# Performance work log

Hardware: AMD Instinct MI355X
Metric: run time of the kernel (lower is better)

The kernel has to match this reference:

```python
import jax, jax.numpy as jnp
import numpy as np

B, L = 64, 200
NQ = 1024          # n_question == output_dim
NPID = 4096
D = 256            # q_embed_dim
H = 512            # hidden_dim
Q = 1024           # output_dim
L2 = 1e-05


def setup_inputs() -> dict:
    key = jax.random.key(0)
    ks = jax.random.split(key, 20)
    q_data = jax.random.randint(ks[0], (B, L), 1, NQ + 1)          # question ids in [1, NQ]
    ans = jax.random.randint(ks[1], (B, L), 0, 2)
    qa_data = q_data + NQ * ans                                     # encoded (q, answer)
    pid_data = jax.random.randint(ks[2], (B, L), 0, NPID + 1)
    matrix = jax.random.uniform(ks[3], (Q, Q), jnp.float32) * 0.05  # p_c_relations
    u = jax.random.uniform(ks[4], (B, L))
    target = jnp.where(u < 0.1, -1.0, jnp.where(u < 0.55, 0.0, 1.0)).astype(jnp.float32)
    s = 0.05
    q_emb = jax.random.normal(ks[5], (NQ + 1, D), jnp.float32) * s
    qa_emb = jax.random.normal(ks[6], (2, D), jnp.float32) * s
    q_emb_diff = jax.random.normal(ks[7], (NQ + 1, D), jnp.float32) * s
    qa_emb_diff = jax.random.normal(ks[8], (2 * NQ + 1, D), jnp.float32) * s
    diff_parm = jax.random.normal(ks[9], (NPID + 1, 1), jnp.float32) * s
    gs = 1.0 / np.sqrt(H).astype(np.float32)
    w_ih = jax.random.uniform(ks[10], (3 * H, 2 * D), jnp.float32, -gs, gs)
    w_hh = jax.random.uniform(ks[11], (3 * H, H), jnp.float32, -gs, gs)
    b_ih = jax.random.uniform(ks[12], (3 * H,), jnp.float32, -gs, gs)
    b_hh = jax.random.uniform(ks[13], (3 * H,), jnp.float32, -gs, gs)
    fc_w = jax.random.normal(ks[14], (Q, H), jnp.float32) * 0.02
    fc_b = jnp.zeros((Q,), jnp.float32)
    return dict(q_data=q_data, qa_data=qa_data, pid_data=pid_data, matrix=matrix,
                target=target, q_emb=q_emb, qa_emb=qa_emb, q_emb_diff=q_emb_diff,
                qa_emb_diff=qa_emb_diff, diff_parm=diff_parm, w_ih=w_ih, w_hh=w_hh,
                b_ih=b_ih, b_hh=b_hh, fc_w=fc_w, fc_b=fc_b)


def _gru(x, w_ih, w_hh, b_ih, b_hh):
    # PyTorch GRU, single layer, batch_first. x: [B, L, In]
    xg = jnp.einsum('bli,gi->blg', x, w_ih) + b_ih          # [B, L, 3H]
    def step(h, xg_t):
        hg = h @ w_hh.T + b_hh
        xr, xz, xn = jnp.split(xg_t, 3, axis=-1)
        hr, hz, hn = jnp.split(hg, 3, axis=-1)
        r = jax.nn.sigmoid(xr + hr)
        z = jax.nn.sigmoid(xz + hz)
        n = jnp.tanh(xn + r * hn)
        h_new = (1.0 - z) * n + z * h
        return h_new, h_new
    h0 = jnp.zeros((x.shape[0], w_hh.shape[1]), x.dtype)
    _, hs = jax.lax.scan(step, h0, xg.transpose(1, 0, 2))
    return hs.transpose(1, 0, 2)                             # [B, L, H]


def reference(q_data, qa_data, pid_data, matrix, target, q_emb, qa_emb,
              q_emb_diff, qa_emb_diff, diff_parm, w_ih, w_hh, b_ih, b_hh,
              fc_w, fc_b):
    q_embed = q_emb[q_data]                                  # [B, L, D]
    qa = (qa_data - q_data) // NQ                            # answer in {0,1}
    qa_embed = qa_emb[qa] + q_embed
    pid_embed = diff_parm[pid_data]                          # [B, L, 1]
    q_embed2 = q_embed + pid_embed * q_emb_diff[q_data]
    qa_embed2 = qa_embed + pid_embed * qa_emb_diff[qa]
    c_reg = (pid_embed ** 2).sum() * L2

    x = jnp.concatenate([qa_embed2, q_embed2], axis=-1)      # [B, L, 2D]
    gru_out = _gru(x, w_ih, w_hh, b_ih, b_hh)
    gru_out = jnp.einsum('blh,qh->blq', gru_out, fc_w) + fc_b  # [B, L, Q]

    got = jnp.einsum('blq,kq->blk', gru_out, matrix)         # [B, L, Q]
    master = jnp.where(got >= 0.4, 1.0, got)                 # threshold-to-1 only
    # mastery of the question asked at step t: master[b, t, q-1]
    mvals = jnp.take_along_axis(master, (q_data - 1)[..., None], axis=2)[..., 0]  # [B, L]

    f32 = jnp.float32
    eq = (q_data[:, :, None] == q_data[:, None, :]).astype(f32)   # [B, t, k]
    t_idx = jnp.arange(L)
    tri_strict = (t_idx[:, None] > t_idx[None, :]).astype(f32)    # k < t
    tri_incl = (t_idx[:, None] >= t_idx[None, :]).astype(f32)     # k <= t
    mast = (mvals == 1.0).astype(f32)
    notm = (mvals == 0.0).astype(f32)
    qa1 = (qa == 1).astype(f32)
    qa0 = 1.0 - qa1
    base = eq * tri_strict                                        # [B, L, L]
    mc = jnp.einsum('btk,bk->bt', base, qa1 * mast)   # master_correct
    mi = jnp.einsum('btk,bk->bt', base, qa0 * mast)   # master_incorrect
    nmc = jnp.einsum('btk,bk->bt', base, qa0 * notm)  # no_master_correct
    aa = jnp.einsum('btk,tk->bt', eq, tri_incl)       # answered_all (>= 1)

    arB = jnp.arange(B)
    idx = q_data - 1

    def dina_step(carry, xs):
        guess, slip = carry                            # [B, Q] each
        i_t, m_t, qa_t, mc_t, mi_t, nmc_t, aa_t = xs   # [B] each
        g_upd = jnp.where(m_t == 1.0, mc_t / aa_t,
                          jnp.where(qa_t == 0, 1.0 - nmc_t / aa_t, nmc_t / aa_t))
        upd_slip = (m_t == 1.0) & (qa_t == 0)
        new_g = jnp.where(upd_slip, guess[arB, i_t], g_upd)
        new_s = jnp.where(upd_slip, mi_t / aa_t, slip[arB, i_t])
        guess = guess.at[arB, i_t].set(new_g)
        slip = slip.at[arB, i_t].set(new_s)
        p = (1.0 - new_s) * (m_t * new_g + (1.0 - new_s) * (1.0 - m_t))
        return (guess, slip), p

    init = (jnp.zeros((B, Q), f32), jnp.zeros((B, Q), f32))
    xs = (idx.T, mvals.T, qa.T, mc.T, mi.T, nmc.T, aa.T)
    _, ps = jax.lax.scan(dina_step, init, xs)          # [L, B]
    preds = ps.T.reshape(-1)                           # [B*L]

    labels = target.reshape(-1)
    mask = labels > -0.9
    preds_d = jax.lax.stop_gradient(preds)             # torch detaches via torch.tensor()
    mse_sum = (((preds_d - labels) ** 2) * mask.astype(f32)).sum()
    loss = mse_sum + c_reg
    return (loss, jax.nn.sigmoid(preds_d), mask.sum())
```

## Files before the change

kernel.cpp:

```cpp
#include <hip/hip_runtime.h>
#include <hip/hip_bf16.h>
#include <math.h>

#define BB 64
#define LL 200
#define NQ 1024
#define DD 256
#define HH 512
#define QQ 1024
#define G3 1536
#define BL 12800
#define GBLK 256

#define OFF_ACC   ((size_t)0)
#define OFF_CELLS ((size_t)16)
#define OFF_HA    ((size_t)1056)
#define OFF_AQ    (OFF_HA + 65536)
#define OFF_DQ    (OFF_AQ + 1574400)
#define OFF_BQA   (OFF_DQ + 1574400)
#define OFF_CQA   (OFF_BQA + 3072)
#define OFF_WSUM  (OFF_CQA + 3072)
#define OFF_FCWT  (OFF_WSUM + 393216)
#define OFF_M2    (OFF_FCWT + 524288)
#define OFF_MB    (OFF_M2 + 524288)
#define OFF_XG    (OFF_MB + 1024)
#define OFF_GRUT  (OFF_XG + 19660800)
#define OFF_QINT  (OFF_GRUT + 6553600)
#define OFF_QAINT (OFF_QINT + 12800)
#define OFF_PIDF  (OFF_QAINT + 12800)
#define OFF_MVAL  (OFF_PIDF + 12800)
#define OFF_MC    (OFF_MVAL + 12800)
#define OFF_MI    (OFF_MC + 12800)
#define OFF_NMC   (OFF_MI + 12800)
#define OFF_AA    (OFF_NMC + 12800)
#define OFF_PREDS (OFF_AA + 12800)

typedef float f32x4 __attribute__((ext_vector_type(4)));

__device__ __forceinline__ float wave_sum64(float v) {
    #pragma unroll
    for (int o = 32; o > 0; o >>= 1) v += __shfl_down(v, o, 64);
    return v;
}

__device__ __forceinline__ f32x4 llc_load4(const float* p) {
    f32x4 v;
    asm volatile("global_load_dwordx4 %0, %1, off sc0 sc1" : "=v"(v) : "v"(p));
    return v;
}
__device__ __forceinline__ void llc_wait2(f32x4& a, f32x4& b) {
    asm volatile("s_waitcnt vmcnt(0)" : "+v"(a), "+v"(b));
}
__device__ __forceinline__ void llc_store1(float* p, float v) {
    asm volatile("global_store_dword %0, %1, off sc0 sc1" :: "v"(p), "v"(v) : "memory");
}

__device__ __forceinline__ float quad_sum(float v) {
    float t1 = __int_as_float(__builtin_amdgcn_update_dpp(
        0, __float_as_int(v), 0xB1, 0xF, 0xF, true));
    v += t1;
    float t2 = __int_as_float(__builtin_amdgcn_update_dpp(
        0, __float_as_int(v), 0x4E, 0xF, 0xF, true));
    return v + t2;
}

__global__ __launch_bounds__(256) void wsum_kernel(const float* __restrict__ w_ih,
                                                   float* __restrict__ wsum)
{
    int g = blockIdx.x, d = threadIdx.x;
    wsum[(size_t)g * DD + d] = w_ih[(size_t)g * 2 * DD + d] + w_ih[(size_t)g * 2 * DD + DD + d];
}

__device__ __forceinline__ void gemm_nt_body(
    const float* __restrict__ A, int lda, const float* __restrict__ B, int ldb,
    float* __restrict__ C, int ldc, int M, int N, int K,
    const float* __restrict__ bias, int bm, int bn, int tid,
    float (*As)[129], float (*Bs)[65])
{
    const int tx = tid & 15, ty = tid >> 4;
    const int mm = tid >> 4, kk = tid & 15;
    float acc[8][4] = {};
    float ar[8], br[4];
    #pragma unroll
    for (int i = 0; i < 8; ++i) {
        int m = bm + mm + 16 * i;
        ar[i] = (m < M) ? A[(size_t)m * lda + kk] : 0.f;
    }
    #pragma unroll
    for (int i = 0; i < 4; ++i) {
        int n = bn + mm + 16 * i;
        br[i] = (n < N) ? B[(size_t)n * ldb + kk] : 0.f;
    }
    for (int k0 = 0; k0 < K; k0 += 16) {
        #pragma unroll
        for (int i = 0; i < 8; ++i) As[kk][mm + 16 * i] = ar[i];
        #pragma unroll
        for (int i = 0; i < 4; ++i) Bs[kk][mm + 16 * i] = br[i];
        __syncthreads();
        int kn = k0 + 16;
        if (kn < K) {
            #pragma unroll
            for (int i = 0; i < 8; ++i) {
                int m = bm + mm + 16 * i;
                ar[i] = (m < M) ? A[(size_t)m * lda + kn + kk] : 0.f;
            }
            #pragma unroll
            for (int i = 0; i < 4; ++i) {
                int n = bn + mm + 16 * i;
                br[i] = (n < N) ? B[(size_t)n * ldb + kn + kk] : 0.f;
            }
        }
        #pragma unroll
        for (int kq = 0; kq < 16; ++kq) {
            float a[8], b[4];
            #pragma unroll
            for (int i = 0; i < 8; ++i) a[i] = As[kq][ty * 8 + i];
            #pragma unroll
            for (int j = 0; j < 4; ++j) b[j] = Bs[kq][tx * 4 + j];
            #pragma unroll
            for (int i = 0; i < 8; ++i)
                #pragma unroll
                for (int j = 0; j < 4; ++j) acc[i][j] += a[i] * b[j];
        }
        __syncthreads();
    }
    #pragma unroll
    for (int i = 0; i < 8; ++i) {
        int m = bm + ty * 8 + i;
        if (m >= M) continue;
        #pragma unroll
        for (int j = 0; j < 4; ++j) {
            int n = bn + tx * 4 + j;
            if (n >= N) continue;
            C[(size_t)m * ldc + n] = acc[i][j] + (bias ? bias[n] : 0.f);
        }
    }
}

__global__ __launch_bounds__(256) void prep_all(
    const float* __restrict__ q_emb, const float* __restrict__ q_emb_diff,
    const float* __restrict__ qa_emb, const float* __restrict__ qa_emb_diff,
    const float* __restrict__ wsum, const float* __restrict__ w_ih,
    const float* __restrict__ b_ih,
    float* __restrict__ Aq, float* __restrict__ Dq,
    float* __restrict__ Bqa, float* __restrict__ Cqa,
    const float* __restrict__ matrix, const float* __restrict__ fc_w,
    const float* __restrict__ fc_b, float* __restrict__ M2, float* __restrict__ mb,
    const int* __restrict__ q_data, const int* __restrict__ qa_data,
    const int* __restrict__ pid_data, const float* __restrict__ diff_parm,
    int* __restrict__ qint, int* __restrict__ qaint, float* __restrict__ pidf,
    float* __restrict__ acc_g)
{
    __shared__ float As[16][129];
    __shared__ float Bs[16][65];
    __shared__ float sm[4];
    const int tid = threadIdx.x;
    const int widx = blockIdx.x;

    if (widx < 432) {
        const int z = widx >= 216;
        const int w2 = z ? widx - 216 : widx;
        const int bm = (w2 / 24) * 128, bn = (w2 % 24) * 64;
        gemm_nt_body(z ? q_emb_diff : q_emb, DD,
                     z ? (w_ih + DD) : wsum, z ? 2 * DD : DD,
                     z ? Dq : Aq, G3, NQ + 1, G3, DD,
                     nullptr, bm, bn, tid, As, Bs);
        return;
    }
    if (widx < 480) {
        const int w2 = widx - 432;
        const int z = w2 >= 24;
        const int bn = (z ? w2 - 24 : w2) * 64;
        gemm_nt_body(z ? qa_emb_diff : qa_emb, DD,
                     w_ih, 2 * DD,
                     z ? Cqa : Bqa, G3, 2, G3, DD,
                     z ? nullptr : b_ih, 0, bn, tid, As, Bs);
        return;
    }
    if (widx < 608) {
        const int w2 = widx - 480;
        const int bm = (w2 >> 3) * 64, bn = (w2 & 7) * 64;
        const int kk = tid & 15, mm = tid >> 4;
        const int nb = tid & 63, kb2 = tid >> 6;
        const int tx = tid & 15, ty = tid >> 4;
        float acc[4][4] = {};
        for (int k0 = 0; k0 < QQ; k0 += 16) {
            if (k0) __syncthreads();
            #pragma unroll
            for (int i = 0; i < 4; ++i)
                As[kk][mm + 16 * i] = matrix[(size_t)(bm + mm + 16 * i) * QQ + k0 + kk];
            #pragma unroll
            for (int i = 0; i < 4; ++i)
                Bs[kb2 + 4 * i][nb] = fc_w[(size_t)(k0 + kb2 + 4 * i) * HH + bn + nb];
            __syncthreads();
            #pragma unroll
            for (int kq = 0; kq < 16; ++kq) {
                float a[4], b[4];
                #pragma unroll
                for (int i = 0; i < 4; ++i) a[i] = As[kq][ty * 4 + i];
                #pragma unroll
                for (int j = 0; j < 4; ++j) b[j] = Bs[kq][tx * 4 + j];
                #pragma unroll
                for (int i = 0; i < 4; ++i)
                    #pragma unroll
                    for (int j = 0; j < 4; ++j) acc[i][j] += a[i] * b[j];
            }
        }
        #pragma unroll
        for (int i = 0; i < 4; ++i)
            #pragma unroll
            for (int j = 0; j < 4; ++j)
                M2[(size_t)(bm + ty * 4 + i) * HH + bn + tx * 4 + j] = acc[i][j];
        return;
    }
    if (widx < 612) {
        const int wv2 = tid >> 6, lane2 = tid & 63;
        const int kb = (widx - 608) * 256 + wv2 * 64;
        for (int i = 0; i < 64; ++i) {
            const float* mrow = matrix + (size_t)(kb + i) * QQ;
            float sacc = 0.f;
            #pragma unroll
            for (int j = 0; j < 16; ++j)
                sacc += mrow[lane2 + 64 * j] * fc_b[lane2 + 64 * j];
            sacc = wave_sum64(sacc);
            if (lane2 == 0) mb[kb + i] = sacc;
        }
        return;
    }
    {
        int r = (widx - 612) * 256 + tid;
        float pp = 0.f;
        if (r < BL) {
            int q = q_data[r];
            qint[r] = q;
            qaint[r] = (qa_data[r] - q) / NQ;
            float pid = diff_parm[pid_data[r]];
            pidf[r] = pid;
            pp = pid * pid;
        }
        pp = wave_sum64(pp);
        int lane = tid & 63, w = tid >> 6;
        if (lane == 0) sm[w] = pp;
        __syncthreads();
        if (tid == 0) atomicAdd(&acc_g[0], sm[0] + sm[1] + sm[2] + sm[3]);
    }
}

__global__ __launch_bounds__(512) void gru_persist(
    const float* __restrict__ Aq,
    const float* __restrict__ Dq,
    const float* __restrict__ Bqa,
    const float* __restrict__ Cqa,
    const int* __restrict__ qint,
    const int* __restrict__ qaint,
    const float* __restrict__ pidf,
    const float* __restrict__ w_hh,
    const float* __restrict__ b_hh,
    float* __restrict__ hA,
    float* __restrict__ gruT2,
    unsigned int* __restrict__ cells)
{
    __shared__ float hs[8][512];
    __shared__ float part[8][3][16][8];
    __shared__ float bqs[2][3][16];
    __shared__ float cqs[2][3][16];
    __shared__ int smq[8][200];
    __shared__ int smqa[8][200];
    __shared__ float smp[8][200];

    const int tid = threadIdx.x;
    const int bid = blockIdx.x;
    const int bg = bid >> 5;
    const int j0 = (bid & 31) * 16;
    const int wv = tid >> 6;
    const int lane = tid & 63;
    const int g = lane >> 2;
    const int s = lane & 3;

    if (tid < 96) {
        const int qa = tid / 48, rem = tid - qa * 48;
        const int gate = rem >> 4, u = rem & 15;
        bqs[qa][gate][u] = Bqa[(size_t)qa * G3 + gate * HH + j0 + u];
        cqs[qa][gate][u] = Cqa[(size_t)qa * G3 + gate * HH + j0 + u];
    }
    for (int i = tid; i < 8 * LL; i += 512) {
        const int c = i / LL, tt = i - c * LL;
        const int col = bg * 8 + c;
        smq[c][tt] = qint[col * LL + tt];
        smqa[c][tt] = qaint[col * LL + tt];
        smp[c][tt] = pidf[col * LL + tt];
    }

    f32x4 ws4[3][4];
    #pragma unroll
    for (int gate = 0; gate < 3; ++gate)
        #pragma unroll
        for (int q = 0; q < 4; ++q)
            ws4[gate][q] = *(const f32x4*)&w_hh[
                (size_t)(gate * HH + j0 + g) * HH + wv * 64 + q * 16 + s * 4];

    const int eu = tid >> 3;
    const int eb = tid & 7;
    float bhr = 0.f, bhz = 0.f, bhn = 0.f;
    if (tid < 128) {
        bhr = b_hh[j0 + eu];
        bhz = b_hh[HH + j0 + eu];
        bhn = b_hh[2 * HH + j0 + eu];
    }

    const int b0 = lane >> 4;
    const int c0 = (lane & 15) * 4;

    __syncthreads();

    for (int t = 0; t < LL; ++t) {
        float xr = 0.f, xz = 0.f, xn = 0.f;
        if (tid < 128) {
            const int q = smq[eb][t];
            const int qa = smqa[eb][t];
            const float pid = smp[eb][t];
            const float* aq = Aq + (size_t)q * G3 + j0 + eu;
            const float* dq = Dq + (size_t)q * G3 + j0 + eu;
            float ar_ = aq[0], az_ = aq[HH], an_ = aq[2 * HH];
            float dr_ = dq[0], dz_ = dq[HH], dn_ = dq[2 * HH];
            xr = ar_ + bqs[qa][0][eu] + pid * (cqs[qa][0][eu] + dr_);
            xz = az_ + bqs[qa][1][eu] + pid * (cqs[qa][1][eu] + dz_);
            xn = an_ + bqs[qa][2][eu] + pid * (cqs[qa][2][eu] + dn_);
        }
        if (t && tid < 64) {
            const unsigned want = (unsigned)t;
            for (;;) {
                unsigned v = want;
                if (lane < 32)
                    v = __hip_atomic_load(&cells[(bg * 32 + lane) * 4],
                                          __ATOMIC_RELAXED, __HIP_MEMORY_SCOPE_AGENT);
                if (__all((int)(v >= want))) break;
                __builtin_amdgcn_s_sleep(2);
            }
        }
        __syncthreads();

        {
            const float* hcur = hA + (size_t)(t & 1) * (HH * BB);
            const float* p0 = hcur + (size_t)(bg * 8 + b0) * HH + wv * 64 + c0;
            f32x4 va = llc_load4(p0);
            f32x4 vb = llc_load4(p0 + 4 * HH);
            llc_wait2(va, vb);
            *(f32x4*)&hs[wv][b0 * 64 + ((c0 + 8 * b0) & 63)] = va;
            *(f32x4*)&hs[wv][(b0 + 4) * 64 + ((c0 + 8 * b0 + 32) & 63)] = vb;
        }

        float acc[3][8];
        #pragma unroll
        for (int gate = 0; gate < 3; ++gate) {
            #pragma unroll
            for (int b = 0; b < 8; ++b) acc[gate][b] = 0.f;
        }
        #pragma unroll
        for (int q = 0; q < 4; ++q) {
            const int cb = q * 16 + s * 4;
            #pragma unroll
            for (int b = 0; b < 8; ++b) {
                f32x4 h4 = *(const f32x4*)&hs[wv][b * 64 + ((cb + 8 * b) & 63)];
                #pragma unroll
                for (int gate = 0; gate < 3; ++gate) {
                    acc[gate][b] += ws4[gate][q].x * h4.x + ws4[gate][q].y * h4.y
                                  + ws4[gate][q].z * h4.z + ws4[gate][q].w * h4.w;
                }
            }
        }

        #pragma unroll
        for (int gate = 0; gate < 3; ++gate)
            #pragma unroll
            for (int b = 0; b < 8; ++b)
                acc[gate][b] = quad_sum(acc[gate][b]);

        if (s < 3) {
            const int rot = (2 * ((g >> 2) + s)) & 7;
            #pragma unroll
            for (int hp = 0; hp < 4; ++hp) {
                const int b = hp * 2;
                float e0 = (s == 0) ? acc[0][b]     : (s == 1) ? acc[1][b]     : acc[2][b];
                float e1 = (s == 0) ? acc[0][b + 1] : (s == 1) ? acc[1][b + 1] : acc[2][b + 1];
                const int bp = (b + rot) & 7;
                *(float2*)&part[wv][s][g][bp] = make_float2(e0, e1);
            }
        }
        __syncthreads();

        if (tid < 128) {
            const int rb = eu >> 2;
            const int bp0 = (eb + 2 * (rb + 0)) & 7;
            const int bp1 = (eb + 2 * (rb + 1)) & 7;
            const int bp2 = (eb + 2 * (rb + 2)) & 7;
            float sg0 = 0.f, sg1 = 0.f, sg2 = 0.f;
            #pragma unroll
            for (int w = 0; w < 8; ++w) {
                sg0 += part[w][0][eu][bp0];
                sg1 += part[w][1][eu][bp1];
                sg2 += part[w][2][eu][bp2];
            }
            const int ku = j0 + eu;
            float hprev = hs[ku >> 6][eb * 64 + (((ku & 63) + 8 * eb) & 63)];
            float rg = 1.f / (1.f + expf(-(xr + sg0 + bhr)));
            float zg = 1.f / (1.f + expf(-(xz + sg1 + bhz)));
            float ng = tanhf(xn + rg * (sg2 + bhn));
            float hn = (1.f - zg) * ng + zg * hprev;
            llc_store1(hA + (size_t)((t + 1) & 1) * (HH * BB)
                          + (size_t)(bg * 8 + eb) * HH + ku, hn);
            gruT2[((size_t)t * BB + bg * 8 + eb) * HH + ku] = hn;
            asm volatile("s_waitcnt vmcnt(0)" ::: "memory");
        }
        __syncthreads();
        if (tid == 0 && t + 1 < LL)
            __hip_atomic_store(&cells[bid * 4], (unsigned)(t + 1),
                               __ATOMIC_RELAXED, __HIP_MEMORY_SCOPE_AGENT);
    }
}

__global__ __launch_bounds__(256) void mval_kernel(
    const float* __restrict__ gruT2,
    const float* __restrict__ M2,
    const float* __restrict__ mb,
    const int* __restrict__ qint,
    float* __restrict__ mval)
{
    int t = blockIdx.x;
    int wave = threadIdx.x >> 6, l = threadIdx.x & 63;
    for (int ii = 0; ii < 16; ++ii) {
        int b = wave * 16 + ii;
        int q = qint[b * LL + t] - 1;
        const float4* hp = (const float4*)(gruT2 + ((size_t)t * BB + b) * HH);
        const float4* mp = (const float4*)(M2 + (size_t)q * HH);
        float4 h0 = hp[l], m0 = mp[l];
        float4 h1 = hp[64 + l], m1 = mp[64 + l];
        float acc = h0.x * m0.x + h0.y * m0.y + h0.z * m0.z + h0.w * m0.w
                  + h1.x * m1.x + h1.y * m1.y + h1.z * m1.z + h1.w * m1.w;
        acc = wave_sum64(acc);
        if (l == 0) {
            float sv = acc + mb[q];
            mval[b * LL + t] = (sv >= 0.4f) ? 1.0f : sv;
        }
    }
}

__global__ __launch_bounds__(256) void statsdina_kernel(
    const int* __restrict__ qint, const int* __restrict__ qaint,
    const float* __restrict__ mval, float* __restrict__ preds)
{
    int b = blockIdx.x, tid = threadIdx.x;
    __shared__ float guess[QQ], slip[QQ];
    __shared__ int qs[LL];
    __shared__ int qas[LL];
    __shared__ float mv[LL], s_mc[LL], s_mi[LL], s_nmc[LL], s_aa[LL];
    for (int i = tid; i < QQ; i += 256) { guess[i] = 0.f; slip[i] = 0.f; }
    if (tid < LL) {
        qs[tid] = qint[b * LL + tid];
        qas[tid] = qaint[b * LL + tid];
        mv[tid] = mval[b * LL + tid];
    }
    __syncthreads();
    if (tid < LL) {
        int qt = qs[tid];
        float smc = 0.f, smi = 0.f, snmc = 0.f, saa = 0.f;
        for (int k = 0; k <= tid; ++k) {
            if (qs[k] == qt) {
                saa += 1.f;
                if (k < tid) {
                    float mk = (mv[k] == 1.f) ? 1.f : 0.f;
                    float nk = (mv[k] == 0.f) ? 1.f : 0.f;
                    float a1 = (qas[k] == 1) ? 1.f : 0.f;
                    smc += a1 * mk;
                    smi += (1.f - a1) * mk;
                    snmc += (1.f - a1) * nk;
                }
            }
        }
        s_mc[tid] = smc;
        s_mi[tid] = smi;
        s_nmc[tid] = snmc;
        s_aa[tid] = saa;
    }
    __syncthreads();
    if (tid == 0) {
        for (int t = 0; t < LL; ++t) {
            int i = qs[t] - 1;
            float m = mv[t];
            int qa = qas[t];
            float aat = s_aa[t];
            float g_upd = (m == 1.f) ? s_mc[t] / aat
                          : ((qa == 0) ? 1.f - s_nmc[t] / aat : s_nmc[t] / aat);
            bool us = (m == 1.f) && (qa == 0);
            float ng = us ? guess[i] : g_upd;
            float ns = us ? s_mi[t] / aat : slip[i];
            guess[i] = ng;
            slip[i] = ns;
            preds[b * LL + t] = (1.f - ns) * (m * ng + (1.f - ns) * (1.f - m));
        }
    }
}

__global__ __launch_bounds__(256) void loss_kernel(
    const float* __restrict__ preds, const float* __restrict__ target,
    float* __restrict__ out, float* __restrict__ acc)
{
    int r = blockIdx.x * 256 + threadIdx.x;
    float lm = 0.f, lc = 0.f;
    if (r < BL) {
        float p = preds[r], lab = target[r];
        float msk = (lab > -0.9f) ? 1.f : 0.f;
        float d = p - lab;
        lm = d * d * msk;
        lc = msk;
        out[1 + r] = 1.f / (1.f + expf(-p));
    }
    lm = wave_sum64(lm);
    lc = wave_sum64(lc);
    __shared__ float sm[4], sc[4];
    int lane = threadIdx.x & 63, w = threadIdx.x >> 6;
    if (lane == 0) { sm[w] = lm; sc[w] = lc; }
    __syncthreads();
    if (threadIdx.x == 0) {
        atomicAdd(&acc[1], sm[0] + sm[1] + sm[2] + sm[3]);
        atomicAdd(&acc[2], sc[0] + sc[1] + sc[2] + sc[3]);
    }
}

__global__ void final_kernel(const float* __restrict__ acc, float* __restrict__ out)
{
    out[0] = acc[1] + acc[0] * 1e-5f;
    out[1 + BL] = acc[2];
}

extern "C" void kernel_launch(void* const* d_in, const int* in_sizes, int n_in,
                              void* d_out, int out_size, void* d_ws, size_t ws_size,
                              hipStream_t stream) {
    const int* q_data = (const int*)d_in[0];
    const int* qa_data = (const int*)d_in[1];
    const int* pid_data = (const int*)d_in[2];
    const float* matrix = (const float*)d_in[3];
    const float* target = (const float*)d_in[4];
    const float* q_emb = (const float*)d_in[5];
    const float* qa_emb = (const float*)d_in[6];
    const float* q_emb_diff = (const float*)d_in[7];
    const float* qa_emb_diff = (const float*)d_in[8];
    const float* diff_parm = (const float*)d_in[9];
    const float* w_ih = (const float*)d_in[10];
    const float* w_hh = (const float*)d_in[11];
    const float* b_ih = (const float*)d_in[12];
    const float* b_hh = (const float*)d_in[13];
    const float* fc_w = (const float*)d_in[14];
    const float* fc_b = (const float*)d_in[15];
    float* out = (float*)d_out;
    float* W = (float*)d_ws;

    float* acc = W + OFF_ACC;
    unsigned int* cells = (unsigned int*)(W + OFF_CELLS);
    float* hA = W + OFF_HA;
    float* Aq = W + OFF_AQ;
    float* Dq = W + OFF_DQ;
    float* Bqa = W + OFF_BQA;
    float* Cqa = W + OFF_CQA;
    float* wsum = W + OFF_WSUM;
    float* M2 = W + OFF_M2;
    float* mb = W + OFF_MB;
    float* gruT2 = W + OFF_GRUT;
    int* qint = (int*)(W + OFF_QINT);
    int* qaint = (int*)(W + OFF_QAINT);
    float* pidf = W + OFF_PIDF;
    float* mval = W + OFF_MVAL;
    float* preds = W + OFF_PREDS;

    hipMemsetAsync(W, 0, (OFF_HA + 2 * HH * BB) * sizeof(float), stream);

    wsum_kernel<<<G3, 256, 0, stream>>>(w_ih, wsum);

    prep_all<<<662, 256, 0, stream>>>(
        q_emb, q_emb_diff, qa_emb, qa_emb_diff, wsum, w_ih, b_ih,
        Aq, Dq, Bqa, Cqa, matrix, fc_w, fc_b, M2, mb,
        q_data, qa_data, pid_data, diff_parm, qint, qaint, pidf, acc);

    gru_persist<<<GBLK, 512, 0, stream>>>(Aq, Dq, Bqa, Cqa, qint, qaint, pidf,
                                          w_hh, b_hh, hA, gruT2, cells);

    mval_kernel<<<LL, 256, 0, stream>>>(gruT2, M2, mb, qint, mval);
    statsdina_kernel<<<BB, 256, 0, stream>>>(qint, qaint, mval, preds);
    loss_kernel<<<50, 256, 0, stream>>>(preds, target, out, acc);
    final_kernel<<<1, 1, 0, stream>>>(acc, out);
}
```

Baseline: 1.075 ms.

## Fuse mval dot-product into persistent GRU kernel, drop gruT2 hidden-state history

Computes each step's mval dot product (previous hidden state against the M2 row for the current question) inside the persistent GRU loop. It uses an otherwise idle wave in the first 8 unit-group blocks and reads the hidden state already staged in shared memory. This removes the full [L,B,H] hidden-state history write and the separate mval kernel launch and its reads. The last timestep needs an extra spin-wait epilogue that waits for all blocks of the batch group before reloading the final state. The cost is extra work on the GRU's critical path and one more cross-block synchronization at the end.

```diff
diff --git a/kernel.cpp b/kernel.cpp
--- a/kernel.cpp
+++ b/kernel.cpp
@@ -257,7 +257,9 @@
     const float* __restrict__ w_hh,
     const float* __restrict__ b_hh,
     float* __restrict__ hA,
-    float* __restrict__ gruT2,
+    const float* __restrict__ M2,
+    const float* __restrict__ mbv,
+    float* __restrict__ mval,
     unsigned int* __restrict__ cells)
 {
     __shared__ float hs[8][512];
@@ -271,7 +273,8 @@
     const int tid = threadIdx.x;
     const int bid = blockIdx.x;
     const int bg = bid >> 5;
-    const int j0 = (bid & 31) * 16;
+    const int ug = bid & 31;
+    const int j0 = ug * 16;
     const int wv = tid >> 6;
     const int lane = tid & 63;
     const int g = lane >> 2;
@@ -389,6 +392,29 @@
         }
         __syncthreads();
 
+        if (wv == 2 && ug < 8 && t >= 1) {
+            const int mvb = ug;
+            const int q = smq[mvb][t - 1] - 1;
+            const float* m2r = M2 + (size_t)q * HH + lane * 8;
+            f32x4 ma = *(const f32x4*)m2r;
+            f32x4 mc4 = *(const f32x4*)(m2r + 4);
+            float sacc = 0.f;
+            #pragma unroll
+            for (int j = 0; j < 8; ++j) {
+                const int k = lane * 8 + j;
+                const float hv = hs[k >> 6][mvb * 64 + (((k & 63) + 8 * mvb) & 63)];
+                const float mvw = (j == 0) ? ma.x : (j == 1) ? ma.y : (j == 2) ? ma.z
+                                : (j == 3) ? ma.w : (j == 4) ? mc4.x : (j == 5) ? mc4.y
+                                : (j == 6) ? mc4.z : mc4.w;
+                sacc += hv * mvw;
+            }
+            sacc = wave_sum64(sacc);
+            if (lane == 0) {
+                float sv = sacc + mbv[q];
+                mval[(bg * 8 + mvb) * LL + (t - 1)] = (sv >= 0.4f) ? 1.0f : sv;
+            }
+        }
+
         if (tid < 128) {
             const int rb = eu >> 2;
             const int bp0 = (eb + 2 * (rb + 0)) & 7;
@@ -409,38 +435,58 @@
             float hn = (1.f - zg) * ng + zg * hprev;
             llc_store1(hA + (size_t)((t + 1) & 1) * (HH * BB)
                           + (size_t)(bg * 8 + eb) * HH + ku, hn);
-            gruT2[((size_t)t * BB + bg * 8 + eb) * HH + ku] = hn;
             asm volatile("s_waitcnt vmcnt(0)" ::: "memory");
         }
         __syncthreads();
-        if (tid == 0 && t + 1 < LL)
+        if (tid == 0)
             __hip_atomic_store(&cells[bid * 4], (unsigned)(t + 1),
                                __ATOMIC_RELAXED, __HIP_MEMORY_SCOPE_AGENT);
     }
-}
-
-__global__ __launch_bounds__(256) void mval_kernel(
-    const float* __restrict__ gruT2,
-    const float* __restrict__ M2,
-    const float* __restrict__ mb,
-    const int* __restrict__ qint,
-    float* __restrict__ mval)
-{
-    int t = blockIdx.x;
-    int wave = threadIdx.x >> 6, l = threadIdx.x & 63;
-    for (int ii = 0; ii < 16; ++ii) {
-        int b = wave * 16 + ii;
-        int q = qint[b * LL + t] - 1;
-        const float4* hp = (const float4*)(gruT2 + ((size_t)t * BB + b) * HH);
-        const float4* mp = (const float4*)(M2 + (size_t)q * HH);
-        float4 h0 = hp[l], m0 = mp[l];
-        float4 h1 = hp[64 + l], m1 = mp[64 + l];
-        float acc = h0.x * m0.x + h0.y * m0.y + h0.z * m0.z + h0.w * m0.w
-                  + h1.x * m1.x + h1.y * m1.y + h1.z * m1.z + h1.w * m1.w;
-        acc = wave_sum64(acc);
-        if (l == 0) {
-            float sv = acc + mb[q];
-            mval[b * LL + t] = (sv >= 0.4f) ? 1.0f : sv;
+
+    if (ug < 8) {
+        if (tid < 64) {
+            const unsigned want = (unsigned)LL;
+            for (;;) {
+                unsigned v = want;
+                if (lane < 32)
+                    v = __hip_atomic_load(&cells[(bg * 32 + lane) * 4],
+                                          __ATOMIC_RELAXED, __HIP_MEMORY_SCOPE_AGENT);
+                if (__all((int)(v >= want))) break;
+                __builtin_amdgcn_s_sleep(2);
+            }
+        }
+        __syncthreads();
+        {
+            const float* hcur = hA + (size_t)(LL & 1) * (HH * BB);
+            const float* p0 = hcur + (size_t)(bg * 8 + b0) * HH + wv * 64 + c0;
+            f32x4 va = llc_load4(p0);
+            f32x4 vb = llc_load4(p0 + 4 * HH);
+            llc_wait2(va, vb);
+            *(f32x4*)&hs[wv][b0 * 64 + ((c0 + 8 * b0) & 63)] = va;
+            *(f32x4*)&hs[wv][(b0 + 4) * 64 + ((c0 + 8 * b0 + 32) & 63)] = vb;
+        }
+        __syncthreads();
+        if (wv == 2) {
+            const int mvb = ug;
+            const int q = smq[mvb][LL - 1] - 1;
+            const float* m2r = M2 + (size_t)q * HH + lane * 8;
+            f32x4 ma = *(const f32x4*)m2r;
+            f32x4 mc4 = *(const f32x4*)(m2r + 4);
+            float sacc = 0.f;
+            #pragma unroll
+            for (int j = 0; j < 8; ++j) {
+                const int k = lane * 8 + j;
+                const float hv = hs[k >> 6][mvb * 64 + (((k & 63) + 8 * mvb) & 63)];
+                const float mvw = (j == 0) ? ma.x : (j == 1) ? ma.y : (j == 2) ? ma.z
+                                : (j == 3) ? ma.w : (j == 4) ? mc4.x : (j == 5) ? mc4.y
+                                : (j == 6) ? mc4.z : mc4.w;
+                sacc += hv * mvw;
+            }
+            sacc = wave_sum64(sacc);
+            if (lane == 0) {
+                float sv = sacc + mbv[q];
+                mval[(bg * 8 + mvb) * LL + (LL - 1)] = (sv >= 0.4f) ? 1.0f : sv;
+            }
         }
     }
 }
@@ -565,7 +611,6 @@
     float* wsum = W + OFF_WSUM;
     float* M2 = W + OFF_M2;
     float* mb = W + OFF_MB;
-    float* gruT2 = W + OFF_GRUT;
     int* qint = (int*)(W + OFF_QINT);
     int* qaint = (int*)(W + OFF_QAINT);
     float* pidf = W + OFF_PIDF;
@@ -582,9 +627,8 @@
         q_data, qa_data, pid_data, diff_parm, qint, qaint, pidf, acc);
 
     gru_persist<<<GBLK, 512, 0, stream>>>(Aq, Dq, Bqa, Cqa, qint, qaint, pidf,
-                                          w_hh, b_hh, hA, gruT2, cells);
-
-    mval_kernel<<<LL, 256, 0, stream>>>(gruT2, M2, mb, qint, mval);
+                                          w_hh, b_hh, hA, M2, mb, mval, cells);
+
     statsdina_kernel<<<BB, 256, 0, stream>>>(qint, qaint, mval, preds);
     loss_kernel<<<50, 256, 0, stream>>>(preds, target, out, acc);
     final_kernel<<<1, 1, 0, stream>>>(acc, out);
```

New measurement: 1.079 ms. No clear change (+0.4%).
